# Kernel tuning notes

Hardware: AMD Instinct MI355X
Metric: run time of the kernel (lower is better)

Reference implementation:

```python
import jax, jax.numpy as jnp
import numpy as np

EPS = 1e-8

def setup_inputs() -> dict:
    key = jax.random.key(0)
    k1, k2 = jax.random.split(key)
    B, C, T_text, max_len = 16, 256, 512, 4096
    x = jax.random.normal(k1, (B, C, T_text), dtype=jnp.float32)
    # positive linear-domain durations, mean ~ max_len / T_text = 8
    w = jax.random.uniform(k2, (B, T_text), dtype=jnp.float32) * 16.0
    x_mask = jnp.ones((B, 1, T_text), dtype=jnp.float32)
    y_mask = jnp.ones((B, 1, max_len), dtype=jnp.float32)
    sigma_scale = jnp.ones((1,), dtype=jnp.float32)
    return {"x": x, "w": w, "x_mask": x_mask, "y_mask": y_mask, "sigma_scale": sigma_scale}

def reference(x, w, x_mask, y_mask, sigma_scale):
    # x: (B, C, T_text), w: (B, T_text), y_mask: (B, 1, max_len)
    x = x * x_mask
    center = jnp.cumsum(w, axis=1) - 0.5 * w            # (B, T_text)
    max_len = y_mask.shape[2]
    pos = jnp.arange(max_len, dtype=x.dtype)            # (max_len,)
    mu = pos[None, None, :] - center[:, :, None]        # (B, T_text, max_len)
    sigma = w[:, :, None] * sigma_scale[0]              # (B, T_text, 1)
    weights = jnp.exp(-0.5 * jnp.square(mu) / (jnp.square(sigma) + EPS))
    weights = weights / (jnp.sum(weights, axis=1, keepdims=True) + EPS)
    upsampled = jnp.einsum('bct,btl->bcl', x, weights)  # (B, C, max_len)
    return upsampled * y_mask
```

## Files before the change

kernel.cpp:

```cpp
#include <hip/hip_runtime.h>
#include <hip/hip_bf16.h>

#define EPS 1e-8f

#define BB 16
#define CC 256
#define TT 512
#define LL 4096
#define KC  32
#define TCB 128
#define TLB 64
#define XR  40

typedef __attribute__((ext_vector_type(8))) short short8;
typedef __attribute__((ext_vector_type(4))) float f32x4;

__device__ __forceinline__ unsigned short bfbits(float f) {
    __hip_bfloat16 h = __float2bfloat16(f);
    return *(unsigned short*)&h;
}
__device__ __forceinline__ unsigned int pack2(float lo, float hi) {
    return (unsigned int)bfbits(lo) | ((unsigned int)bfbits(hi) << 16);
}


#define EXPW(tc_, buf_)                                                         \
    {                                                                           \
        const int l_loc = tid >> 2;                                             \
        const int tg    = tid & 3;                                              \
        const int t0    = (tc_) + tg * 8;                                       \
        const float4 cv0 = *(const float4*)&cen_s[t0];                          \
        const float4 cv1 = *(const float4*)&cen_s[t0 + 4];                      \
        const float4 nv0 = *(const float4*)&nh_s[t0];                           \
        const float4 nv1 = *(const float4*)&nh_s[t0 + 4];                       \
        const float4 xk0 = *(const float4*)&xm_s[t0];                           \
        const float4 xk1 = *(const float4*)&xm_s[t0 + 4];                       \
        const float posf = (float)(l0 + l_loc);                                 \
        float mu, e0, e1, e2, e3, e4, e5, e6, e7;                               \
        mu = posf - cv0.x; e0 = __expf(mu * mu * nv0.x);                        \
        mu = posf - cv0.y; e1 = __expf(mu * mu * nv0.y);                        \
        mu = posf - cv0.z; e2 = __expf(mu * mu * nv0.z);                        \
        mu = posf - cv0.w; e3 = __expf(mu * mu * nv0.w);                        \
        mu = posf - cv1.x; e4 = __expf(mu * mu * nv1.x);                        \
        mu = posf - cv1.y; e5 = __expf(mu * mu * nv1.y);                        \
        mu = posf - cv1.z; e6 = __expf(mu * mu * nv1.z);                        \
        mu = posf - cv1.w; e7 = __expf(mu * mu * nv1.w);                        \
        p0 += ((e0 + e1) + (e2 + e3)) + ((e4 + e5) + (e6 + e7));                \
        uint4 pk;                                                               \
        pk.x = pack2(e0 * xk0.x, e1 * xk0.y);                                   \
        pk.y = pack2(e2 * xk0.z, e3 * xk0.w);                                   \
        pk.z = pack2(e4 * xk1.x, e5 * xk1.y);                                   \
        pk.w = pack2(e6 * xk1.z, e7 * xk1.w);                                   \
        *(uint4*)&ws[buf_][l_loc][tg * 8] = pk;                                 \
    }

#define AFRAG(AF, crow_, tc_)                                                   \
    {                                                                           \
        const float* xp = &x[xbase + (size_t)(crow_) * TT + (tc_) + lg * 8];    \
        const float4 a0 = *(const float4*)xp;                                   \
        const float4 a1 = *(const float4*)(xp + 4);                             \
        uint4 ap;                                                               \
        ap.x = pack2(a0.x, a0.y);                                               \
        ap.y = pack2(a0.z, a0.w);                                               \
        ap.z = pack2(a1.x, a1.y);                                               \
        ap.w = pack2(a1.z, a1.w);                                               \
        AF = *(short8*)&ap;                                                     \
    }

#define MFMA_STEP(buf_, tc_)                                                    \
    {                                                                           \
        short8 af0, af1;                                                        \
        AFRAG(af0, wv * 32 + lq, tc_);                                          \
        AFRAG(af1, wv * 32 + 16 + lq, tc_);                                     \
        _Pragma("unroll")                                                       \
        for (int n = 0; n < 4; ++n) {                                           \
            const short8 bfr = *(const short8*)&ws[buf_][n * 16 + lq][lg * 8];  \
            acc0[n] = __builtin_amdgcn_mfma_f32_16x16x32_bf16(af0, bfr, acc0[n], 0, 0, 0); \
            acc1[n] = __builtin_amdgcn_mfma_f32_16x16x32_bf16(af1, bfr, acc1[n], 0, 0, 0); \
        }                                                                       \
    }

__global__ __launch_bounds__(256, 4)
void fused_kernel(const float* __restrict__ x,
                  const float* __restrict__ w,
                  const float* __restrict__ x_mask,
                  const float* __restrict__ y_mask,
                  const float* __restrict__ sigma_scale,
                  float* __restrict__ out) {
    __shared__ unsigned short ws[2][TLB][XR];
    __shared__ float cen_s[TT], nh_s[TT], xm_s[TT];
    __shared__ float dsum[TLB], sscale[TLB];
    __shared__ float part[4], offs[4];
    __shared__ int tmin_s, tmax_s;

    const int gid = blockIdx.x;
    const int lid = (gid & 7) * 256 + (gid >> 3);
    const int b   = lid >> 7;
    const int rr  = lid & 127;
    const int l0  = (rr >> 1) * TLB;
    const int c0  = (rr & 1) * TCB;

    const int tid  = threadIdx.x;
    const int lane = tid & 63;
    const int wid  = tid >> 6;
    const int wv   = wid;
    const int lq   = lane & 15;
    const int lg   = lane >> 4;
    const int bTT  = b * TT;
    const size_t xbase = (size_t)(b * CC + c0) * TT;

    if (tid == 0) { tmin_s = TT; tmax_s = -1; }

    const int t2 = tid * 2;
    const float2 w2  = *(const float2*)&w[bTT + t2];
    const float2 xm2 = *(const float2*)&x_mask[bTT + t2];
    const float ss = sigma_scale[0];
    const float pairsum = w2.x + w2.y;
    float v = pairsum;
#pragma unroll
    for (int o = 1; o < 64; o <<= 1) {
        float u = __shfl_up(v, o);
        if (lane >= o) v += u;
    }
    if (lane == 63) part[wid] = v;
    __syncthreads();
    if (tid == 0) {
        float run = 0.0f;
#pragma unroll
        for (int i = 0; i < 4; ++i) { offs[i] = run; run += part[i]; }
    }
    __syncthreads();
    const float base = offs[wid] + v - pairsum;
    const float cum1 = base + w2.x;
    const float cum2 = cum1 + w2.y;
    const float cenA = cum1 - 0.5f * w2.x;
    const float cenB = cum2 - 0.5f * w2.y;
    cen_s[t2]     = cenA;
    cen_s[t2 + 1] = cenB;
    const float sgA = w2.x * ss, sgB = w2.y * ss;
    nh_s[t2]     = -0.5f / (sgA * sgA + EPS);
    nh_s[t2 + 1] = -0.5f / (sgB * sgB + EPS);
    xm_s[t2]     = xm2.x;
    xm_s[t2 + 1] = xm2.y;

    const float l0f = (float)l0;
    const float l1f = l0f + (float)(TLB - 1);
    const float rA = 8.0f * sgA + 1.0f;
    const float rB = 8.0f * sgB + 1.0f;
    if (cenA + rA >= l0f && cenA - rA <= l1f) {
        atomicMin(&tmin_s, t2); atomicMax(&tmax_s, t2);
    }
    if (cenB + rB >= l0f && cenB - rB <= l1f) {
        atomicMin(&tmin_s, t2 + 1); atomicMax(&tmax_s, t2 + 1);
    }
    __syncthreads();
    const int tlo = tmin_s & ~(KC - 1);
    const int nch = (tmax_s >= 0) ? ((((tmax_s & ~(KC - 1)) + KC) - tlo) / KC) : 0;

    f32x4 acc0[4], acc1[4];
#pragma unroll
    for (int n = 0; n < 4; ++n) { acc0[n] = (f32x4)0.0f; acc1[n] = (f32x4)0.0f; }
    float p0 = 0.0f;

    if (nch > 0) {
        EXPW(tlo, 0);
        __syncthreads();
        for (int i = 0; i < nch; ++i) {
            const int cur = i & 1;
            if (i + 1 < nch) EXPW(tlo + (i + 1) * KC, cur ^ 1);
            MFMA_STEP(cur, tlo + i * KC);
            __syncthreads();
        }
    }

    p0 += __shfl_xor(p0, 1); p0 += __shfl_xor(p0, 2);
    if ((tid & 3) == 0) dsum[tid >> 2] = p0;
    __syncthreads();
    if (tid < TLB)
        sscale[tid] = y_mask[b * LL + l0 + tid] / (dsum[tid] + EPS);
    __syncthreads();

    float sc[4];
#pragma unroll
    for (int n = 0; n < 4; ++n) sc[n] = sscale[n * 16 + lq];

    const size_t obase = (size_t)(b * CC + c0) * LL + l0;
#pragma unroll
    for (int r = 0; r < 4; ++r) {
        const int cA = wv * 32 + lg * 4 + r;
        float* opA = &out[obase + (size_t)cA * LL];
#pragma unroll
        for (int n = 0; n < 4; ++n) opA[n * 16 + lq] = acc0[n][r] * sc[n];
        float* opB = opA + 16 * LL;
#pragma unroll
        for (int n = 0; n < 4; ++n) opB[n * 16 + lq] = acc1[n][r] * sc[n];
    }
}

extern "C" void kernel_launch(void* const* d_in, const int* in_sizes, int n_in,
                              void* d_out, int out_size, void* d_ws, size_t ws_size,
                              hipStream_t stream) {
    const float* x           = (const float*)d_in[0];
    const float* w           = (const float*)d_in[1];
    const float* x_mask      = (const float*)d_in[2];
    const float* y_mask      = (const float*)d_in[3];
    const float* sigma_scale = (const float*)d_in[4];
    float* out = (float*)d_out;

    hipLaunchKernelGGL(fused_kernel, dim3((LL / TLB) * (CC / TCB) * BB), dim3(256), 0, stream,
                       x, w, x_mask, y_mask, sigma_scale, out);
}
```

Before: 25.08 us.

## Hoist per-batch scan into separate kernel and halve L tile size

Moves the cumsum and the per-token center, inverse-variance and radius computation into a small pre-kernel that writes to workspace, so each main block no longer rescans all 512 durations. The L tile shrinks from 64 to 32, doubling the grid and giving each block a tighter range of contributing tokens. The truncation radius narrows from 8 sigma to 6.5 sigma, and the chunk start is no longer aligned to KC, which trims the chunk count further. The cost is an extra kernel launch, more redundant x-fragment loads per output column, and unaligned global float4 reads of cen/nh/x_mask.

```diff
diff --git a/kernel.cpp b/kernel.cpp
--- a/kernel.cpp
+++ b/kernel.cpp
@@ -9,7 +9,7 @@
 #define LL 4096
 #define KC  32
 #define TCB 128
-#define TLB 64
+#define TLB 32
 #define XR  40
 
 typedef __attribute__((ext_vector_type(8))) short short8;
@@ -23,35 +23,59 @@
     return (unsigned int)bfbits(lo) | ((unsigned int)bfbits(hi) << 16);
 }
 
+__global__ __launch_bounds__(512)
+void scan_kernel(const float* __restrict__ w,
+                 const float* __restrict__ sigma_scale,
+                 float* __restrict__ cenG,
+                 float* __restrict__ nhG,
+                 float* __restrict__ radG) {
+    const int b = blockIdx.x;
+    const int t = threadIdx.x;
+    const int lane = t & 63;
+    const int wid  = t >> 6;
+    __shared__ float part[8], offs[8];
+
+    const float wv = w[b * TT + t];
+    float v = wv;
+#pragma unroll
+    for (int o = 1; o < 64; o <<= 1) {
+        float u = __shfl_up(v, o);
+        if (lane >= o) v += u;
+    }
+    if (lane == 63) part[wid] = v;
+    __syncthreads();
+    if (t == 0) {
+        float run = 0.0f;
+#pragma unroll
+        for (int i = 0; i < 8; ++i) { offs[i] = run; run += part[i]; }
+    }
+    __syncthreads();
+    const float cum = offs[wid] + v;
+    const float ss  = sigma_scale[0];
+    const float sg  = wv * ss;
+    cenG[b * TT + t] = cum - 0.5f * wv;
+    nhG[b * TT + t]  = -0.5f / (sg * sg + EPS);
+    radG[b * TT + t] = 6.5f * sg + 1.0f;
+}
+
 
 #define EXPW(tc_, buf_)                                                         \
     {                                                                           \
-        const int l_loc = tid >> 2;                                             \
-        const int tg    = tid & 3;                                              \
-        const int t0    = (tc_) + tg * 8;                                       \
-        const float4 cv0 = *(const float4*)&cen_s[t0];                          \
-        const float4 cv1 = *(const float4*)&cen_s[t0 + 4];                      \
-        const float4 nv0 = *(const float4*)&nh_s[t0];                           \
-        const float4 nv1 = *(const float4*)&nh_s[t0 + 4];                       \
-        const float4 xk0 = *(const float4*)&xm_s[t0];                           \
-        const float4 xk1 = *(const float4*)&xm_s[t0 + 4];                       \
+        const int t0 = (tc_) + tg * 4;                                          \
+        const float4 cv = *(const float4*)&cenG[bTT + t0];                      \
+        const float4 nv = *(const float4*)&nhG[bTT + t0];                       \
+        const float4 xk = *(const float4*)&x_mask[bTT + t0];                    \
         const float posf = (float)(l0 + l_loc);                                 \
-        float mu, e0, e1, e2, e3, e4, e5, e6, e7;                               \
-        mu = posf - cv0.x; e0 = __expf(mu * mu * nv0.x);                        \
-        mu = posf - cv0.y; e1 = __expf(mu * mu * nv0.y);                        \
-        mu = posf - cv0.z; e2 = __expf(mu * mu * nv0.z);                        \
-        mu = posf - cv0.w; e3 = __expf(mu * mu * nv0.w);                        \
-        mu = posf - cv1.x; e4 = __expf(mu * mu * nv1.x);                        \
-        mu = posf - cv1.y; e5 = __expf(mu * mu * nv1.y);                        \
-        mu = posf - cv1.z; e6 = __expf(mu * mu * nv1.z);                        \
-        mu = posf - cv1.w; e7 = __expf(mu * mu * nv1.w);                        \
-        p0 += ((e0 + e1) + (e2 + e3)) + ((e4 + e5) + (e6 + e7));                \
-        uint4 pk;                                                               \
-        pk.x = pack2(e0 * xk0.x, e1 * xk0.y);                                   \
-        pk.y = pack2(e2 * xk0.z, e3 * xk0.w);                                   \
-        pk.z = pack2(e4 * xk1.x, e5 * xk1.y);                                   \
-        pk.w = pack2(e6 * xk1.z, e7 * xk1.w);                                   \
-        *(uint4*)&ws[buf_][l_loc][tg * 8] = pk;                                 \
+        float mu, e0, e1, e2, e3;                                               \
+        mu = posf - cv.x; e0 = __expf(mu * mu * nv.x);                          \
+        mu = posf - cv.y; e1 = __expf(mu * mu * nv.y);                          \
+        mu = posf - cv.z; e2 = __expf(mu * mu * nv.z);                          \
+        mu = posf - cv.w; e3 = __expf(mu * mu * nv.w);                          \
+        p += (e0 + e1) + (e2 + e3);                                             \
+        uint2 pk;                                                               \
+        pk.x = pack2(e0 * xk.x, e1 * xk.y);                                     \
+        pk.y = pack2(e2 * xk.z, e3 * xk.w);                                     \
+        *(uint2*)&ws[buf_][l_loc][tg * 4] = pk;                                 \
     }
 
 #define AFRAG(AF, crow_, tc_)                                                   \
@@ -70,10 +94,10 @@
 #define MFMA_STEP(buf_, tc_)                                                    \
     {                                                                           \
         short8 af0, af1;                                                        \
-        AFRAG(af0, wv * 32 + lq, tc_);                                          \
-        AFRAG(af1, wv * 32 + 16 + lq, tc_);                                     \
+        AFRAG(af0, wid * 32 + lq, tc_);                                         \
+        AFRAG(af1, wid * 32 + 16 + lq, tc_);                                    \
         _Pragma("unroll")                                                       \
-        for (int n = 0; n < 4; ++n) {                                           \
+        for (int n = 0; n < 2; ++n) {                                           \
             const short8 bfr = *(const short8*)&ws[buf_][n * 16 + lq][lg * 8];  \
             acc0[n] = __builtin_amdgcn_mfma_f32_16x16x32_bf16(af0, bfr, acc0[n], 0, 0, 0); \
             acc1[n] = __builtin_amdgcn_mfma_f32_16x16x32_bf16(af1, bfr, acc1[n], 0, 0, 0); \
@@ -82,85 +106,61 @@
 
 __global__ __launch_bounds__(256, 4)
 void fused_kernel(const float* __restrict__ x,
-                  const float* __restrict__ w,
                   const float* __restrict__ x_mask,
                   const float* __restrict__ y_mask,
-                  const float* __restrict__ sigma_scale,
+                  const float* __restrict__ cenG,
+                  const float* __restrict__ nhG,
+                  const float* __restrict__ radG,
                   float* __restrict__ out) {
     __shared__ unsigned short ws[2][TLB][XR];
-    __shared__ float cen_s[TT], nh_s[TT], xm_s[TT];
     __shared__ float dsum[TLB], sscale[TLB];
-    __shared__ float part[4], offs[4];
     __shared__ int tmin_s, tmax_s;
 
     const int gid = blockIdx.x;
-    const int lid = (gid & 7) * 256 + (gid >> 3);
-    const int b   = lid >> 7;
-    const int rr  = lid & 127;
+    const int lid = (gid & 7) * 512 + (gid >> 3);
+    const int b   = lid >> 8;
+    const int rr  = lid & 255;
     const int l0  = (rr >> 1) * TLB;
     const int c0  = (rr & 1) * TCB;
 
     const int tid  = threadIdx.x;
     const int lane = tid & 63;
     const int wid  = tid >> 6;
-    const int wv   = wid;
     const int lq   = lane & 15;
     const int lg   = lane >> 4;
+    const int l_loc = tid >> 3;
+    const int tg    = tid & 7;
     const int bTT  = b * TT;
     const size_t xbase = (size_t)(b * CC + c0) * TT;
 
     if (tid == 0) { tmin_s = TT; tmax_s = -1; }
-
-    const int t2 = tid * 2;
-    const float2 w2  = *(const float2*)&w[bTT + t2];
-    const float2 xm2 = *(const float2*)&x_mask[bTT + t2];
-    const float ss = sigma_scale[0];
-    const float pairsum = w2.x + w2.y;
-    float v = pairsum;
-#pragma unroll
-    for (int o = 1; o < 64; o <<= 1) {
-        float u = __shfl_up(v, o);
-        if (lane >= o) v += u;
-    }
-    if (lane == 63) part[wid] = v;
-    __syncthreads();
-    if (tid == 0) {
-        float run = 0.0f;
-#pragma unroll
-        for (int i = 0; i < 4; ++i) { offs[i] = run; run += part[i]; }
-    }
-    __syncthreads();
-    const float base = offs[wid] + v - pairsum;
-    const float cum1 = base + w2.x;
-    const float cum2 = cum1 + w2.y;
-    const float cenA = cum1 - 0.5f * w2.x;
-    const float cenB = cum2 - 0.5f * w2.y;
-    cen_s[t2]     = cenA;
-    cen_s[t2 + 1] = cenB;
-    const float sgA = w2.x * ss, sgB = w2.y * ss;
-    nh_s[t2]     = -0.5f / (sgA * sgA + EPS);
-    nh_s[t2 + 1] = -0.5f / (sgB * sgB + EPS);
-    xm_s[t2]     = xm2.x;
-    xm_s[t2 + 1] = xm2.y;
+    __syncthreads();
 
     const float l0f = (float)l0;
     const float l1f = l0f + (float)(TLB - 1);
-    const float rA = 8.0f * sgA + 1.0f;
-    const float rB = 8.0f * sgB + 1.0f;
-    if (cenA + rA >= l0f && cenA - rA <= l1f) {
-        atomicMin(&tmin_s, t2); atomicMax(&tmax_s, t2);
-    }
-    if (cenB + rB >= l0f && cenB - rB <= l1f) {
-        atomicMin(&tmin_s, t2 + 1); atomicMax(&tmax_s, t2 + 1);
-    }
-    __syncthreads();
-    const int tlo = tmin_s & ~(KC - 1);
-    const int nch = (tmax_s >= 0) ? ((((tmax_s & ~(KC - 1)) + KC) - tlo) / KC) : 0;
-
-    f32x4 acc0[4], acc1[4];
-#pragma unroll
-    for (int n = 0; n < 4; ++n) { acc0[n] = (f32x4)0.0f; acc1[n] = (f32x4)0.0f; }
-    float p0 = 0.0f;
+#pragma unroll
+    for (int i = 0; i < 2; ++i) {
+        const int tt = tid + 256 * i;
+        const float cen = cenG[bTT + tt];
+        const float rad = radG[bTT + tt];
+        if (cen + rad >= l0f && cen - rad <= l1f) {
+            atomicMin(&tmin_s, tt);
+            atomicMax(&tmax_s, tt);
+        }
+    }
+    __syncthreads();
+
+    int nch = 0, tlo = 0;
+    if (tmax_s >= 0) {
+        nch = (tmax_s - tmin_s + KC) / KC;
+        tlo = tmin_s;
+        if (tlo + nch * KC > TT) tlo = TT - nch * KC;
+    }
+
+    f32x4 acc0[2], acc1[2];
+#pragma unroll
+    for (int n = 0; n < 2; ++n) { acc0[n] = (f32x4)0.0f; acc1[n] = (f32x4)0.0f; }
+    float p = 0.0f;
 
     if (nch > 0) {
         EXPW(tlo, 0);
@@ -173,27 +173,27 @@
         }
     }
 
-    p0 += __shfl_xor(p0, 1); p0 += __shfl_xor(p0, 2);
-    if ((tid & 3) == 0) dsum[tid >> 2] = p0;
+    p += __shfl_xor(p, 1);
+    p += __shfl_xor(p, 2);
+    p += __shfl_xor(p, 4);
+    if ((lane & 7) == 0) dsum[wid * 8 + (lane >> 3)] = p;
     __syncthreads();
     if (tid < TLB)
         sscale[tid] = y_mask[b * LL + l0 + tid] / (dsum[tid] + EPS);
     __syncthreads();
 
-    float sc[4];
-#pragma unroll
-    for (int n = 0; n < 4; ++n) sc[n] = sscale[n * 16 + lq];
-
+    const float sc0 = sscale[lq];
+    const float sc1 = sscale[16 + lq];
     const size_t obase = (size_t)(b * CC + c0) * LL + l0;
 #pragma unroll
     for (int r = 0; r < 4; ++r) {
-        const int cA = wv * 32 + lg * 4 + r;
-        float* opA = &out[obase + (size_t)cA * LL];
-#pragma unroll
-        for (int n = 0; n < 4; ++n) opA[n * 16 + lq] = acc0[n][r] * sc[n];
+        const int rowA = wid * 32 + lg * 4 + r;
+        float* opA = &out[obase + (size_t)rowA * LL];
+        opA[lq]      = acc0[0][r] * sc0;
+        opA[16 + lq] = acc0[1][r] * sc1;
         float* opB = opA + 16 * LL;
-#pragma unroll
-        for (int n = 0; n < 4; ++n) opB[n * 16 + lq] = acc1[n][r] * sc[n];
+        opB[lq]      = acc1[0][r] * sc0;
+        opB[16 + lq] = acc1[1][r] * sc1;
     }
 }
 
@@ -207,6 +207,13 @@
     const float* sigma_scale = (const float*)d_in[4];
     float* out = (float*)d_out;
 
-    hipLaunchKernelGGL(fused_kernel, dim3((LL / TLB) * (CC / TCB) * BB), dim3(256), 0, stream,
-                       x, w, x_mask, y_mask, sigma_scale, out);
-}
+    float* cenG = (float*)d_ws;
+    float* nhG  = cenG + BB * TT;
+    float* radG = nhG + BB * TT;
+
+    hipLaunchKernelGGL(scan_kernel, dim3(BB), dim3(512), 0, stream,
+                       w, sigma_scale, cenG, nhG, radG);
+    hipLaunchKernelGGL(fused_kernel,
+                       dim3((LL / TLB) * (CC / TCB) * BB), dim3(256), 0, stream,
+                       x, x_mask, y_mask, cenG, nhG, radG, out);
+}
```

After: 28.76 us. +14.7%, slower.

## Hoist prefix scan and window bounds into a separate per-batch pre-kernel

Applied to the files above, without the earlier changes.

Moves the cumsum, the center/inverse-variance computation and the per-window active-token range search out of every fused block into a small scan kernel that runs once per batch row. Each fused block then only loads the precomputed arrays and its own range. The cut-off radius shrinks from 8 sigma to 6.5 sigma, and the chunk start is aligned to 4 instead of 32, so fewer chunks are processed. In exchange there is a second kernel launch plus a global-memory round trip, and the tighter cut-off drops slightly more of each Gaussian tail.

```diff
diff --git a/kernel.cpp b/kernel.cpp
--- a/kernel.cpp
+++ b/kernel.cpp
@@ -10,6 +10,7 @@
 #define KC  32
 #define TCB 128
 #define TLB 64
+#define NW  (LL / TLB)
 #define XR  40
 
 typedef __attribute__((ext_vector_type(8))) short short8;
@@ -23,12 +24,62 @@
     return (unsigned int)bfbits(lo) | ((unsigned int)bfbits(hi) << 16);
 }
 
+__global__ __launch_bounds__(512)
+void scan_kernel(const float* __restrict__ w,
+                 const float* __restrict__ sigma_scale,
+                 float* __restrict__ cenG,
+                 float* __restrict__ nhG,
+                 int* __restrict__ tmnG,
+                 int* __restrict__ tmxG) {
+    const int b = blockIdx.x;
+    const int t = threadIdx.x;
+    const int lane = t & 63;
+    const int wid  = t >> 6;
+    __shared__ float part[8], offs[8];
+
+    if (t < NW) { tmnG[b * NW + t] = TT; tmxG[b * NW + t] = -1; }
+
+    const float wv = w[b * TT + t];
+    float v = wv;
+#pragma unroll
+    for (int o = 1; o < 64; o <<= 1) {
+        float u = __shfl_up(v, o);
+        if (lane >= o) v += u;
+    }
+    if (lane == 63) part[wid] = v;
+    __syncthreads();
+    if (t == 0) {
+        float run = 0.0f;
+#pragma unroll
+        for (int i = 0; i < 8; ++i) { offs[i] = run; run += part[i]; }
+    }
+    __syncthreads();
+    const float cum = offs[wid] + v;
+    const float ss  = sigma_scale[0];
+    const float sg  = wv * ss;
+    const float cen = cum - 0.5f * wv;
+    const float rad = 6.5f * sg + 1.0f;
+    cenG[b * TT + t] = cen;
+    nhG[b * TT + t]  = -0.5f / (sg * sg + EPS);
+
+    int wlo = (int)floorf((cen - rad) * (1.0f / TLB)) - 1;
+    int whi = (int)floorf((cen + rad) * (1.0f / TLB)) + 1;
+    if (wlo < 0) wlo = 0;
+    if (whi > NW - 1) whi = NW - 1;
+    for (int wi = wlo; wi <= whi; ++wi) {
+        const float w0 = (float)(wi * TLB);
+        const float w1 = w0 + (float)(TLB - 1);
+        if (cen + rad >= w0 && cen - rad <= w1) {
+            atomicMin(&tmnG[b * NW + wi], t);
+            atomicMax(&tmxG[b * NW + wi], t);
+        }
+    }
+}
+
 
 #define EXPW(tc_, buf_)                                                         \
     {                                                                           \
-        const int l_loc = tid >> 2;                                             \
-        const int tg    = tid & 3;                                              \
-        const int t0    = (tc_) + tg * 8;                                       \
+        const int t0 = (tc_) + tg * 8;                                          \
         const float4 cv0 = *(const float4*)&cen_s[t0];                          \
         const float4 cv1 = *(const float4*)&cen_s[t0 + 4];                      \
         const float4 nv0 = *(const float4*)&nh_s[t0];                           \
@@ -45,7 +96,7 @@
         mu = posf - cv1.y; e5 = __expf(mu * mu * nv1.y);                        \
         mu = posf - cv1.z; e6 = __expf(mu * mu * nv1.z);                        \
         mu = posf - cv1.w; e7 = __expf(mu * mu * nv1.w);                        \
-        p0 += ((e0 + e1) + (e2 + e3)) + ((e4 + e5) + (e6 + e7));                \
+        p += ((e0 + e1) + (e2 + e3)) + ((e4 + e5) + (e6 + e7));                 \
         uint4 pk;                                                               \
         pk.x = pack2(e0 * xk0.x, e1 * xk0.y);                                   \
         pk.y = pack2(e2 * xk0.z, e3 * xk0.w);                                   \
@@ -70,8 +121,8 @@
 #define MFMA_STEP(buf_, tc_)                                                    \
     {                                                                           \
         short8 af0, af1;                                                        \
-        AFRAG(af0, wv * 32 + lq, tc_);                                          \
-        AFRAG(af1, wv * 32 + 16 + lq, tc_);                                     \
+        AFRAG(af0, wid * 32 + lq, tc_);                                         \
+        AFRAG(af1, wid * 32 + 16 + lq, tc_);                                    \
         _Pragma("unroll")                                                       \
         for (int n = 0; n < 4; ++n) {                                           \
             const short8 bfr = *(const short8*)&ws[buf_][n * 16 + lq][lg * 8];  \
@@ -82,16 +133,16 @@
 
 __global__ __launch_bounds__(256, 4)
 void fused_kernel(const float* __restrict__ x,
-                  const float* __restrict__ w,
                   const float* __restrict__ x_mask,
                   const float* __restrict__ y_mask,
-                  const float* __restrict__ sigma_scale,
+                  const float* __restrict__ cenG,
+                  const float* __restrict__ nhG,
+                  const int* __restrict__ tmnG,
+                  const int* __restrict__ tmxG,
                   float* __restrict__ out) {
     __shared__ unsigned short ws[2][TLB][XR];
     __shared__ float cen_s[TT], nh_s[TT], xm_s[TT];
     __shared__ float dsum[TLB], sscale[TLB];
-    __shared__ float part[4], offs[4];
-    __shared__ int tmin_s, tmax_s;
 
     const int gid = blockIdx.x;
     const int lid = (gid & 7) * 256 + (gid >> 3);
@@ -103,64 +154,37 @@
     const int tid  = threadIdx.x;
     const int lane = tid & 63;
     const int wid  = tid >> 6;
-    const int wv   = wid;
     const int lq   = lane & 15;
     const int lg   = lane >> 4;
+    const int l_loc = tid >> 2;
+    const int tg    = tid & 3;
     const int bTT  = b * TT;
     const size_t xbase = (size_t)(b * CC + c0) * TT;
 
-    if (tid == 0) { tmin_s = TT; tmax_s = -1; }
-
-    const int t2 = tid * 2;
-    const float2 w2  = *(const float2*)&w[bTT + t2];
-    const float2 xm2 = *(const float2*)&x_mask[bTT + t2];
-    const float ss = sigma_scale[0];
-    const float pairsum = w2.x + w2.y;
-    float v = pairsum;
-#pragma unroll
-    for (int o = 1; o < 64; o <<= 1) {
-        float u = __shfl_up(v, o);
-        if (lane >= o) v += u;
-    }
-    if (lane == 63) part[wid] = v;
-    __syncthreads();
-    if (tid == 0) {
-        float run = 0.0f;
-#pragma unroll
-        for (int i = 0; i < 4; ++i) { offs[i] = run; run += part[i]; }
-    }
-    __syncthreads();
-    const float base = offs[wid] + v - pairsum;
-    const float cum1 = base + w2.x;
-    const float cum2 = cum1 + w2.y;
-    const float cenA = cum1 - 0.5f * w2.x;
-    const float cenB = cum2 - 0.5f * w2.y;
-    cen_s[t2]     = cenA;
-    cen_s[t2 + 1] = cenB;
-    const float sgA = w2.x * ss, sgB = w2.y * ss;
-    nh_s[t2]     = -0.5f / (sgA * sgA + EPS);
-    nh_s[t2 + 1] = -0.5f / (sgB * sgB + EPS);
-    xm_s[t2]     = xm2.x;
-    xm_s[t2 + 1] = xm2.y;
-
-    const float l0f = (float)l0;
-    const float l1f = l0f + (float)(TLB - 1);
-    const float rA = 8.0f * sgA + 1.0f;
-    const float rB = 8.0f * sgB + 1.0f;
-    if (cenA + rA >= l0f && cenA - rA <= l1f) {
-        atomicMin(&tmin_s, t2); atomicMax(&tmax_s, t2);
-    }
-    if (cenB + rB >= l0f && cenB - rB <= l1f) {
-        atomicMin(&tmin_s, t2 + 1); atomicMax(&tmax_s, t2 + 1);
-    }
-    __syncthreads();
-    const int tlo = tmin_s & ~(KC - 1);
-    const int nch = (tmax_s >= 0) ? ((((tmax_s & ~(KC - 1)) + KC) - tlo) / KC) : 0;
+#pragma unroll
+    for (int i = 0; i < 2; ++i) {
+        const int tt = tid + 256 * i;
+        cen_s[tt] = cenG[bTT + tt];
+        nh_s[tt]  = nhG[bTT + tt];
+        xm_s[tt]  = x_mask[bTT + tt];
+    }
+    const int widx = b * NW + (l0 / TLB);
+    const int tmn = tmnG[widx];
+    const int tmx = tmxG[widx];
+    __syncthreads();
+
+    int nch = 0, tlo = 0;
+    if (tmx >= 0) {
+        tlo = tmn & ~3;
+        nch = (tmx - tlo + KC) / KC;
+        const int maxlo = TT - nch * KC;
+        if (tlo > maxlo) tlo = maxlo;
+    }
 
     f32x4 acc0[4], acc1[4];
 #pragma unroll
     for (int n = 0; n < 4; ++n) { acc0[n] = (f32x4)0.0f; acc1[n] = (f32x4)0.0f; }
-    float p0 = 0.0f;
+    float p = 0.0f;
 
     if (nch > 0) {
         EXPW(tlo, 0);
@@ -173,8 +197,9 @@
         }
     }
 
-    p0 += __shfl_xor(p0, 1); p0 += __shfl_xor(p0, 2);
-    if ((tid & 3) == 0) dsum[tid >> 2] = p0;
+    p += __shfl_xor(p, 1);
+    p += __shfl_xor(p, 2);
+    if (tg == 0) dsum[l_loc] = p;
     __syncthreads();
     if (tid < TLB)
         sscale[tid] = y_mask[b * LL + l0 + tid] / (dsum[tid] + EPS);
@@ -187,8 +212,8 @@
     const size_t obase = (size_t)(b * CC + c0) * LL + l0;
 #pragma unroll
     for (int r = 0; r < 4; ++r) {
-        const int cA = wv * 32 + lg * 4 + r;
-        float* opA = &out[obase + (size_t)cA * LL];
+        const int rowA = wid * 32 + lg * 4 + r;
+        float* opA = &out[obase + (size_t)rowA * LL];
 #pragma unroll
         for (int n = 0; n < 4; ++n) opA[n * 16 + lq] = acc0[n][r] * sc[n];
         float* opB = opA + 16 * LL;
@@ -207,6 +232,14 @@
     const float* sigma_scale = (const float*)d_in[4];
     float* out = (float*)d_out;
 
-    hipLaunchKernelGGL(fused_kernel, dim3((LL / TLB) * (CC / TCB) * BB), dim3(256), 0, stream,
-                       x, w, x_mask, y_mask, sigma_scale, out);
-}
+    float* cenG = (float*)d_ws;
+    float* nhG  = cenG + BB * TT;
+    int*   tmnG = (int*)(nhG + BB * TT);
+    int*   tmxG = tmnG + BB * NW;
+
+    hipLaunchKernelGGL(scan_kernel, dim3(BB), dim3(512), 0, stream,
+                       w, sigma_scale, cenG, nhG, tmnG, tmxG);
+    hipLaunchKernelGGL(fused_kernel,
+                       dim3((LL / TLB) * (CC / TCB) * BB), dim3(256), 0, stream,
+                       x, x_mask, y_mask, cenG, nhG, tmnG, tmxG, out);
+}
```

After: 31.94 us. 1.27x slower.
